# Kernel tuning notes

Hardware: AMD Instinct MI355X
Metric: run time of the kernel (lower is better)

The kernel has to match this reference:

```python
import jax, jax.numpy as jnp
import numpy as np

N = 50000      # nodes
E = 800000     # edges (before self-loops)
G = 128        # graphs in batch
IN = 128       # in_channels
HID = 32       # hidden_channels (per head)
HEADS = 4
OUT = 64       # out_channels
SLOPE = 0.2    # PyG GATConv default negative_slope


def setup_inputs() -> dict:
    key = jax.random.key(0)
    ks = jax.random.split(key, 24)
    s = 0.1
    inp = {
        'x': jax.random.normal(ks[0], (N, IN), jnp.float32),
        'edge_index': jax.random.randint(ks[1], (2, E), 0, N, dtype=jnp.int32),
        'batch': jnp.sort(jax.random.randint(ks[2], (N,), 0, G, dtype=jnp.int32)),
        # conv1: IN -> HEADS*HID, concat
        'W1': jax.random.normal(ks[3], (IN, HEADS * HID), jnp.float32) * s,
        'a1s': jax.random.normal(ks[4], (HEADS, HID), jnp.float32) * s,
        'a1d': jax.random.normal(ks[5], (HEADS, HID), jnp.float32) * s,
        'b1': jnp.zeros((HEADS * HID,), jnp.float32),
        # conv2: HEADS*HID -> HEADS*HID, concat
        'W2': jax.random.normal(ks[6], (HEADS * HID, HEADS * HID), jnp.float32) * s,
        'a2s': jax.random.normal(ks[7], (HEADS, HID), jnp.float32) * s,
        'a2d': jax.random.normal(ks[8], (HEADS, HID), jnp.float32) * s,
        'b2': jnp.zeros((HEADS * HID,), jnp.float32),
        # conv3
        'W3': jax.random.normal(ks[9], (HEADS * HID, HEADS * HID), jnp.float32) * s,
        'a3s': jax.random.normal(ks[10], (HEADS, HID), jnp.float32) * s,
        'a3d': jax.random.normal(ks[11], (HEADS, HID), jnp.float32) * s,
        'b3': jnp.zeros((HEADS * HID,), jnp.float32),
        # conv4: heads=1, concat=False -> HID
        'W4': jax.random.normal(ks[12], (HEADS * HID, 1 * HID), jnp.float32) * s,
        'a4s': jax.random.normal(ks[13], (1, HID), jnp.float32) * s,
        'a4d': jax.random.normal(ks[14], (1, HID), jnp.float32) * s,
        'b4': jnp.zeros((HID,), jnp.float32),
        # fc: HID -> OUT
        'fcW': jax.random.normal(ks[15], (HID, OUT), jnp.float32) * s,
        'fcb': jnp.zeros((OUT,), jnp.float32),
    }
    return inp


def gat_conv(x, src, dst, W, a_src, a_dst, bias, heads, ch, concat):
    # x: [N, F_in]; src/dst: [E'] with self-loops (PyG add_self_loops=True)
    h = (x @ W).reshape(N, heads, ch)                       # [N, H, C]
    alpha_s = jnp.einsum('nhc,hc->nh', h, a_src)            # [N, H]
    alpha_d = jnp.einsum('nhc,hc->nh', h, a_dst)
    e = jax.nn.leaky_relu(alpha_s[src] + alpha_d[dst], SLOPE)  # [E', H]
    # segment softmax over edges grouped by destination node
    e_max = jax.ops.segment_max(e, dst, num_segments=N)
    e = jnp.exp(e - e_max[dst])
    denom = jax.ops.segment_sum(e, dst, num_segments=N)
    alpha = e / (denom[dst] + 1e-16)                        # [E', H]
    msg = h[src] * alpha[:, :, None]                        # [E', H, C]
    out = jax.ops.segment_sum(msg, dst, num_segments=N)     # [N, H, C]
    out = out.reshape(N, heads * ch) if concat else out.mean(axis=1)
    return out + bias


def reference(x, edge_index, batch, W1, a1s, a1d, b1, W2, a2s, a2d, b2,
              W3, a3s, a3d, b3, W4, a4s, a4d, b4, fcW, fcb):
    loop = jnp.arange(N, dtype=edge_index.dtype)
    src = jnp.concatenate([edge_index[0], loop])            # add self-loops once
    dst = jnp.concatenate([edge_index[1], loop])
    h = jax.nn.elu(gat_conv(x, src, dst, W1, a1s, a1d, b1, HEADS, HID, True))
    h = jax.nn.elu(gat_conv(h, src, dst, W2, a2s, a2d, b2, HEADS, HID, True))
    h = jax.nn.elu(gat_conv(h, src, dst, W3, a3s, a3d, b3, HEADS, HID, True))
    h = jax.nn.elu(gat_conv(h, src, dst, W4, a4s, a4d, b4, 1, HID, False))
    # global mean pool over graphs
    counts = jax.ops.segment_sum(jnp.ones((N,), h.dtype), batch, num_segments=G)
    pooled = jax.ops.segment_sum(h, batch, num_segments=G) / jnp.maximum(counts, 1.0)[:, None]
    # dropout p=0.5 is identity at inference
    return pooled @ fcW + fcb                               # [G, OUT]
```

## Files before the change

kernel.cpp:

```cpp
#include <hip/hip_runtime.h>


constexpr int NN     = 50000;
constexpr int NNPAD  = 50048;
constexpr int EE     = 800000;
constexpr int ETOT   = EE + NN;
constexpr int GG     = 128;
constexpr int HIDC   = 32;
constexpr int OUTC   = 64;

constexpr int NRANGE = (NN + 127) / 128;
constexpr int EPB    = 4096;
constexpr int NBLK   = (EE + EPB - 1) / EPB;
constexpr int RCAP   = 2688;

typedef short  bf16x8 __attribute__((ext_vector_type(8)));
typedef float  f32x4  __attribute__((ext_vector_type(4)));

static __device__ __forceinline__ unsigned short f2bf(float f) {
    unsigned int u = __float_as_uint(f);
    unsigned int r = (u + 0x7fffu + ((u >> 16) & 1u)) >> 16;
    return (unsigned short)r;
}
static __device__ __forceinline__ float bflo(unsigned int v) {
    return __uint_as_float(v << 16);
}
static __device__ __forceinline__ float bfhi(unsigned int v) {
    return __uint_as_float(v & 0xffff0000u);
}

__global__ __launch_bounds__(256) void local_sort_kernel(
    const int* __restrict__ ei,
    unsigned int* __restrict__ blocksorted,
    int* __restrict__ boffs)
{
    __shared__ unsigned int sorted[EPB];
    __shared__ int hist[NRANGE + 1];
    __shared__ int scanv[NRANGE + 1];
    __shared__ int cur[NRANGE + 1];
    __shared__ int wsum4[4];
    __shared__ int ct_s;

    const int b = blockIdx.x, tid = threadIdx.x;
    const int lane = tid & 63, wid = tid >> 6;
    const int e0 = b * EPB;
    const int ecnt = min(EPB, EE - e0);

    for (int t = tid; t < NRANGE + 1; t += 256) hist[t] = 0;
    __syncthreads();

    unsigned int recs[16];
    int rkey[16];
#pragma unroll
    for (int k = 0; k < 16; ++k) {
        const int idx = tid + k * 256;
        rkey[k] = -1;
        if (idx < ecnt) {
            const int src = ei[e0 + idx];
            const int dst = ei[EE + e0 + idx];
            const int r = dst >> 7;
            recs[k] = (unsigned int)src | ((unsigned int)(dst & 127) << 16);
            rkey[k] = r;
            atomicAdd(&hist[r], 1);
        }
    }
    __syncthreads();

    int carry = 0;
    for (int base = 0; base < NRANGE + 1; base += 256) {
        const int i = base + tid;
        const int v = (i < NRANGE + 1) ? hist[i] : 0;
        int incl = v;
#pragma unroll
        for (int off = 1; off < 64; off <<= 1) {
            int t = __shfl_up(incl, off, 64);
            if (lane >= off) incl += t;
        }
        if (lane == 63) wsum4[wid] = incl;
        __syncthreads();
        if (tid == 0) {
            int s = 0;
#pragma unroll
            for (int w = 0; w < 4; ++w) { int t = wsum4[w]; wsum4[w] = s; s += t; }
            ct_s = s;
        }
        __syncthreads();
        const int excl = carry + wsum4[wid] + incl - v;
        if (i < NRANGE + 1) { scanv[i] = excl; cur[i] = excl; }
        carry += ct_s;
        __syncthreads();
    }

#pragma unroll
    for (int k = 0; k < 16; ++k) {
        if (rkey[k] >= 0) {
            const int pos = atomicAdd(&cur[rkey[k]], 1);
            sorted[pos] = recs[k];
        }
    }
    __syncthreads();

    for (int t = tid; t < ecnt; t += 256)
        blocksorted[(size_t)b * EPB + t] = sorted[t];
    for (int t = tid; t < NRANGE + 1; t += 256)
        boffs[b * (NRANGE + 1) + t] = scanv[t];
}

__global__ __launch_bounds__(512) void rbase_kernel(const int* __restrict__ boffs,
                                                    int* __restrict__ rbase)
{
    __shared__ int wsum[8], wpre[8];
    const int tid = threadIdx.x, lane = tid & 63, wid = tid >> 6;
    int tot = 0;
    if (tid < NRANGE) {
        for (int b = 0; b < NBLK; ++b) {
            const int* bp = boffs + b * (NRANGE + 1) + tid;
            tot += bp[1] - bp[0];
        }
        tot += min(128, NN - tid * 128);
    }
    int incl = tot;
#pragma unroll
    for (int off = 1; off < 64; off <<= 1) {
        int t = __shfl_up(incl, off, 64);
        if (lane >= off) incl += t;
    }
    if (lane == 63) wsum[wid] = incl;
    __syncthreads();
    if (tid < 8) {
        int wv = wsum[tid], winc = wv;
#pragma unroll
        for (int off = 1; off < 8; off <<= 1) {
            int t = __shfl_up(winc, off, 64);
            if (tid >= off) winc += t;
        }
        wpre[tid] = winc - wv;
    }
    __syncthreads();
    const int excl = wpre[wid] + incl - tot;
    if (tid < NRANGE) rbase[tid] = excl;
    if (tid == NRANGE - 1) rbase[NRANGE] = excl + tot;
}

__global__ __launch_bounds__(256) void phaseB_kernel(
    const int* __restrict__ boffs,
    const unsigned int* __restrict__ blocksorted,
    const int* __restrict__ rbase,
    int* __restrict__ offs,
    int* __restrict__ csrsrc)
{
    __shared__ unsigned int   rec[RCAP];
    __shared__ unsigned short outsrc[RCAP];
    __shared__ int runoff[NBLK + 1];
    __shared__ int bstart[NBLK];
    __shared__ int hist[128], lofs[128], cur[128];
    __shared__ int wsum4[4];
    __shared__ int tot0_s;

    const int r = blockIdx.x, tid = threadIdx.x;
    const int lane = tid & 63, wid = tid >> 6;
    const int base = r * 128;
    const int rn   = min(128, NN - base);

    int cnt = 0;
    if (tid < NBLK) {
        const int* bp = boffs + tid * (NRANGE + 1) + r;
        const int s = bp[0];
        bstart[tid] = s;
        cnt = bp[1] - s;
    }
    if (tid < 128) hist[tid] = 0;
    int incl = cnt;
#pragma unroll
    for (int off = 1; off < 64; off <<= 1) {
        int t = __shfl_up(incl, off, 64);
        if (lane >= off) incl += t;
    }
    if (lane == 63) wsum4[wid] = incl;
    __syncthreads();
    if (tid == 0) {
        int s = 0;
#pragma unroll
        for (int w = 0; w < 4; ++w) { int t = wsum4[w]; wsum4[w] = s; s += t; }
    }
    __syncthreads();
    const int excl = wsum4[wid] + incl - cnt;
    if (tid <= NBLK) runoff[tid] = excl;
    __syncthreads();

    const int tot8 = runoff[NBLK];
    for (int i = tid; i < tot8; i += 256) {
        int lo = 0, hi = NBLK;
        while (lo + 1 < hi) {
            const int mid = (lo + hi) >> 1;
            if (runoff[mid] <= i) lo = mid; else hi = mid;
        }
        rec[i] = blocksorted[(size_t)lo * EPB + bstart[lo] + (i - runoff[lo])];
    }
    for (int t = tid; t < rn; t += 256)
        rec[tot8 + t] = (unsigned int)(base + t) | ((unsigned int)t << 16);
    const int total = min(tot8 + rn, RCAP);
    __syncthreads();

    for (int t = tid; t < total; t += 256) atomicAdd(&hist[rec[t] >> 16], 1);
    __syncthreads();

    if (tid < 64) {
        int v = hist[tid], incl2 = v;
#pragma unroll
        for (int off = 1; off < 64; off <<= 1) {
            int t = __shfl_up(incl2, off, 64);
            if (tid >= off) incl2 += t;
        }
        lofs[tid] = incl2 - v;
        if (tid == 63) tot0_s = incl2;
    }
    __syncthreads();
    if (tid >= 64 && tid < 128) {
        const int l = tid & 63;
        int v = hist[tid], incl2 = v;
#pragma unroll
        for (int off = 1; off < 64; off <<= 1) {
            int t = __shfl_up(incl2, off, 64);
            if (l >= off) incl2 += t;
        }
        lofs[tid] = tot0_s + incl2 - v;
    }
    __syncthreads();

    if (tid < 128) cur[tid] = lofs[tid];
    if (tid < rn) offs[base + tid] = rbase[r] + lofs[tid];
    if (r == 0 && tid == 0) offs[NN] = rbase[NRANGE];
    __syncthreads();

    for (int t = tid; t < total; t += 256) {
        const unsigned int rc = rec[t];
        const int pos = atomicAdd(&cur[rc >> 16], 1);
        outsrc[pos] = (unsigned short)(rc & 0xffffu);
    }
    __syncthreads();
    const int rb = rbase[r];
    for (int t = tid; t < total; t += 256) csrsrc[rb + t] = (int)outsrc[t];
}

__global__ __launch_bounds__(256) void prep_kernel(
    const float* __restrict__ W1, const float* __restrict__ a1s, const float* __restrict__ a1d,
    const float* __restrict__ W2, const float* __restrict__ a2s, const float* __restrict__ a2d,
    const float* __restrict__ W3, const float* __restrict__ a3s, const float* __restrict__ a3d,
    const float* __restrict__ W4, const float* __restrict__ a4s, const float* __restrict__ a4d,
    unsigned short* __restrict__ wtg)
{
    __shared__ float ahat_s[128 * 8];
    const int l = blockIdx.x, tid = threadIdx.x;
    const float *W, *as_, *ad_;
    int fo, nh;
    if (l == 0)      { W = W1; as_ = a1s; ad_ = a1d; fo = 128; nh = 4; }
    else if (l == 1) { W = W2; as_ = a2s; ad_ = a2d; fo = 128; nh = 4; }
    else if (l == 2) { W = W3; as_ = a3s; ad_ = a3d; fo = 128; nh = 4; }
    else             { W = W4; as_ = a4s; ad_ = a4d; fo = 32;  nh = 1; }
    const int F_STG = fo + 16;

    for (int item = tid; item < 128 * 8; item += 256) {
        const int k = item >> 3, j = item & 7;
        const int hh = j & 3;
        const bool is_d = j >= 4;
        float v = 0.f;
        if (hh < nh) {
            const float* av = (is_d ? ad_ : as_) + hh * 32;
            const float* wp = W + (size_t)k * fo + hh * 32;
#pragma unroll 8
            for (int c = 0; c < 32; ++c) v = fmaf(wp[c], av[c], v);
        }
        ahat_s[item] = v;
    }
    __syncthreads();

    unsigned short* outb = wtg + (size_t)l * (144 * 128);
    for (int p = tid; p < F_STG * 64; p += 256) {
        const int n  = p % F_STG;
        const int k2 = p / F_STG;
        float w0 = 0.f, w1 = 0.f;
        if (n < fo) {
            w0 = W[(size_t)(2 * k2) * fo + n];
            w1 = W[(size_t)(2 * k2 + 1) * fo + n];
        } else {
            const int j = n - fo;
            if (j < 8) {
                w0 = ahat_s[(2 * k2) * 8 + j];
                w1 = ahat_s[(2 * k2 + 1) * 8 + j];
            }
        }
        const unsigned int packed = (unsigned int)f2bf(w0) | ((unsigned int)f2bf(w1) << 16);
        const int byte = n * 256 + ((4 * k2) ^ ((n & 7) << 4));
        *reinterpret_cast<unsigned int*>(reinterpret_cast<char*>(outb) + byte) = packed;
    }
}

__global__ void convert_x_kernel(const float* __restrict__ x, unsigned short* __restrict__ xb)
{
    int i = blockIdx.x * blockDim.x + threadIdx.x;
    if (i >= (NNPAD * 128) / 2) return;
    unsigned int packed = 0;
    if (2 * i < NN * 128) {
        float f0 = x[2 * i], f1 = x[2 * i + 1];
        packed = (unsigned int)f2bf(f0) | ((unsigned int)f2bf(f1) << 16);
    }
    reinterpret_cast<unsigned int*>(xb)[i] = packed;
}

template<int F_OUT, int NH>
__global__ __launch_bounds__(256) void gemm_mfma_kernel(
    const unsigned short* __restrict__ xb,
    const unsigned short* __restrict__ wtg,
    unsigned short* __restrict__ hb,
    float* __restrict__ as_out, float* __restrict__ ad_out)
{
    constexpr int F_STG = F_OUT + 16;
    __shared__ unsigned short wt[F_STG * 128];
    const int tid = threadIdx.x;

    {
        const bf16x8* __restrict__ wg = reinterpret_cast<const bf16x8*>(wtg);
        bf16x8* wl = reinterpret_cast<bf16x8*>(wt);
        constexpr int NV = F_STG * 16;
#pragma unroll
        for (int i = 0; i < NV / 256; ++i)
            wl[i * 256 + tid] = wg[i * 256 + tid];
    }
    __syncthreads();

    const int wave = tid >> 6, lane = tid & 63;
    const int row0 = blockIdx.x * 64 + wave * 16;
    const int arow = row0 + (lane & 15);
    const int kchunk = (lane >> 4) * 8;

    const unsigned short* __restrict__ ap = xb + (size_t)arow * 128;
    bf16x8 a[4];
#pragma unroll
    for (int ks = 0; ks < 4; ++ks)
        a[ks] = *reinterpret_cast<const bf16x8*>(ap + ks * 32 + kchunk);

    const int kb_base = (lane >> 4) * 16;
    const int rbase = row0 + (lane >> 4) * 4;

#pragma unroll
    for (int nt = 0; nt < F_OUT / 16; ++nt) {
        const int n = nt * 16 + (lane & 15);
        f32x4 acc = {0.f, 0.f, 0.f, 0.f};
#pragma unroll
        for (int ks = 0; ks < 4; ++ks) {
            const int byte = n * 256 + ((ks * 64 + kb_base) ^ ((n & 7) << 4));
            bf16x8 b = *reinterpret_cast<const bf16x8*>(
                reinterpret_cast<const char*>(wt) + byte);
            acc = __builtin_amdgcn_mfma_f32_16x16x32_bf16(a[ks], b, acc, 0, 0, 0);
        }
#pragma unroll
        for (int r = 0; r < 4; ++r)
            hb[(size_t)(rbase + r) * F_OUT + n] = f2bf(acc[r]);
    }

    {
        const int n = F_OUT + (lane & 15);
        f32x4 acc = {0.f, 0.f, 0.f, 0.f};
#pragma unroll
        for (int ks = 0; ks < 4; ++ks) {
            const int byte = n * 256 + ((ks * 64 + kb_base) ^ ((n & 7) << 4));
            bf16x8 b = *reinterpret_cast<const bf16x8*>(
                reinterpret_cast<const char*>(wt) + byte);
            acc = __builtin_amdgcn_mfma_f32_16x16x32_bf16(a[ks], b, acc, 0, 0, 0);
        }
        const int col = lane & 15;
        if (col < 8) {
            const int hh = col & 3;
            const bool is_d = col >= 4;
            if (hh < NH) {
                float* op = is_d ? ad_out : as_out;
#pragma unroll
                for (int r = 0; r < 4; ++r) {
                    const int row = rbase + r;
                    if (row < NN) {
                        if (NH == 4) op[row * 4 + hh] = acc[r];
                        else         op[row]          = acc[r];
                    }
                }
            }
        }
    }
}

template<int HEADS, int F_OUT, bool OUT_BF16>
__global__ __launch_bounds__(256) void aggregate_kernel(
    const unsigned short* __restrict__ hlin,
    const float* __restrict__ as_,
    const float* __restrict__ ad_,
    const int* __restrict__ offs,
    const int* __restrict__ csr_src,
    const float* __restrict__ bias,
    void* __restrict__ out_v)
{
    __shared__ float w_all[4][64 * HEADS];
    __shared__ int   s_all[4][64];
    const int wave = threadIdx.x >> 6;
    const int lane = threadIdx.x & 63;
    const int d    = blockIdx.x * 4 + wave;
    if (d >= NN) return;
    float* __restrict__ w_lds  = w_all[wave];
    int*   __restrict__ src_lds = s_all[wave];

    const int beg  = offs[d], end = offs[d + 1];
    const int deg  = end - beg;

    float ad_h[HEADS];
#pragma unroll
    for (int h = 0; h < HEADS; ++h) ad_h[h] = ad_[d * HEADS + h];

    float inv[HEADS];

    if (deg <= 64) {
        float ex[HEADS];
#pragma unroll
        for (int h = 0; h < HEADS; ++h) ex[h] = 0.f;
        int src = 0;
        if (lane < deg) {
            src = csr_src[beg + lane];
            if (HEADS == 4) {
                const float4 av = *reinterpret_cast<const float4*>(as_ + (size_t)src * 4);
                const float avv[4] = {av.x, av.y, av.z, av.w};
#pragma unroll
                for (int h = 0; h < 4; ++h) {
                    float e = avv[h] + ad_h[h];
                    e = fmaxf(e, 0.f) + 0.2f * fminf(e, 0.f);
                    ex[h] = __expf(e);
                }
            } else {
                float e = as_[src] + ad_h[0];
                e = fmaxf(e, 0.f) + 0.2f * fminf(e, 0.f);
                ex[0] = __expf(e);
            }
        }
        src_lds[lane] = src;
#pragma unroll
        for (int h = 0; h < HEADS; ++h) {
            float s = ex[h];
#pragma unroll
            for (int k = 1; k < 64; k <<= 1) s += __shfl_xor(s, k, 64);
            inv[h] = 1.f / (s + 1e-16f);
            w_lds[lane * HEADS + h] = ex[h] * inv[h];
        }
        asm volatile("s_waitcnt lgkmcnt(0)" ::: "memory");
    } else {
        float ssum[HEADS];
#pragma unroll
        for (int h = 0; h < HEADS; ++h) ssum[h] = 0.f;
        for (int p = beg + lane; p < end; p += 64) {
            const int src = csr_src[p];
            if (HEADS == 4) {
                const float4 av = *reinterpret_cast<const float4*>(as_ + (size_t)src * 4);
                const float avv[4] = {av.x, av.y, av.z, av.w};
#pragma unroll
                for (int h = 0; h < 4; ++h) {
                    float e = avv[h] + ad_h[h];
                    e = fmaxf(e, 0.f) + 0.2f * fminf(e, 0.f);
                    ssum[h] += __expf(e);
                }
            } else {
                float e = as_[src] + ad_h[0];
                e = fmaxf(e, 0.f) + 0.2f * fminf(e, 0.f);
                ssum[0] += __expf(e);
            }
        }
#pragma unroll
        for (int h = 0; h < HEADS; ++h) {
            float s = ssum[h];
#pragma unroll
            for (int k = 1; k < 64; k <<= 1) s += __shfl_xor(s, k, 64);
            inv[h] = 1.f / (s + 1e-16f);
        }
    }

    float acc[4] = {0.f, 0.f, 0.f, 0.f};

    for (int base = beg; base < end; base += 64) {
        const int cnt = min(64, end - base);
        if (deg > 64) {
            const int p = base + lane;
            int src = 0;
            float w[HEADS];
#pragma unroll
            for (int h = 0; h < HEADS; ++h) w[h] = 0.f;
            if (p < end) {
                src = csr_src[p];
                if (HEADS == 4) {
                    const float4 av = *reinterpret_cast<const float4*>(as_ + (size_t)src * 4);
                    const float avv[4] = {av.x, av.y, av.z, av.w};
#pragma unroll
                    for (int h = 0; h < 4; ++h) {
                        float e = avv[h] + ad_h[h];
                        e = fmaxf(e, 0.f) + 0.2f * fminf(e, 0.f);
                        w[h] = __expf(e) * inv[h];
                    }
                } else {
                    float e = as_[src] + ad_h[0];
                    e = fmaxf(e, 0.f) + 0.2f * fminf(e, 0.f);
                    w[0] = __expf(e) * inv[0];
                }
            }
            src_lds[lane] = src;
#pragma unroll
            for (int h = 0; h < HEADS; ++h) w_lds[lane * HEADS + h] = w[h];
            asm volatile("s_waitcnt lgkmcnt(0)" ::: "memory");
        }

        if (F_OUT == 128) {
            const int half = lane >> 5, cl = lane & 31;
            const int cntR = (cnt + 1) & ~1;
#pragma unroll 4
            for (int j = 0; j < cntR; j += 2) {
                const int   srcj = src_lds[j + half];
                const float w    = w_lds[(j + half) * 4 + (cl >> 3)];
                const uint2 hv   = *reinterpret_cast<const uint2*>(
                    hlin + (size_t)srcj * 128 + cl * 4);
                acc[0] = fmaf(w, bflo(hv.x), acc[0]);
                acc[1] = fmaf(w, bfhi(hv.x), acc[1]);
                acc[2] = fmaf(w, bflo(hv.y), acc[2]);
                acc[3] = fmaf(w, bfhi(hv.y), acc[3]);
            }
        } else {
            const int q = lane >> 4, cl = lane & 15;
            const int cntR = (cnt + 3) & ~3;
#pragma unroll 4
            for (int j = 0; j < cntR; j += 4) {
                const int   srcj = src_lds[j + q];
                const float w    = w_lds[j + q];
                const unsigned int hv = *reinterpret_cast<const unsigned int*>(
                    hlin + (size_t)srcj * 32 + cl * 2);
                acc[0] = fmaf(w, bflo(hv), acc[0]);
                acc[1] = fmaf(w, bfhi(hv), acc[1]);
            }
        }
    }

    if (F_OUT == 128) {
#pragma unroll
        for (int t = 0; t < 4; ++t) acc[t] += __shfl_xor(acc[t], 32, 64);
        if (lane < 32) {
            const int c0 = lane * 4;
            float v[4];
#pragma unroll
            for (int t = 0; t < 4; ++t) {
                float v0 = acc[t] + bias[c0 + t];
                v[t] = (v0 > 0.f) ? v0 : (__expf(v0) - 1.f);
            }
            unsigned int p0 = (unsigned int)f2bf(v[0]) | ((unsigned int)f2bf(v[1]) << 16);
            unsigned int p1 = (unsigned int)f2bf(v[2]) | ((unsigned int)f2bf(v[3]) << 16);
            uint2* op = reinterpret_cast<uint2*>(
                (unsigned short*)out_v + (size_t)d * 128 + c0);
            *op = make_uint2(p0, p1);
        }
    } else {
        acc[0] += __shfl_xor(acc[0], 16, 64); acc[0] += __shfl_xor(acc[0], 32, 64);
        acc[1] += __shfl_xor(acc[1], 16, 64); acc[1] += __shfl_xor(acc[1], 32, 64);
        if (lane < 16) {
            const int c0 = lane * 2;
            float v0 = acc[0] + bias[c0];
            float v1 = acc[1] + bias[c0 + 1];
            v0 = (v0 > 0.f) ? v0 : (__expf(v0) - 1.f);
            v1 = (v1 > 0.f) ? v1 : (__expf(v1) - 1.f);
            if (OUT_BF16) {
                unsigned int pk = (unsigned int)f2bf(v0) | ((unsigned int)f2bf(v1) << 16);
                reinterpret_cast<unsigned int*>(out_v)[(size_t)d * 16 + lane] = pk;
            } else {
                reinterpret_cast<float2*>(out_v)[(size_t)d * 16 + lane] =
                    make_float2(v0, v1);
            }
        }
    }
}

__global__ __launch_bounds__(256) void pool_fc_kernel(
    const float* __restrict__ h4, const int* __restrict__ batch,
    const float* __restrict__ fcW, const float* __restrict__ fcb,
    float* __restrict__ out)
{
    const int g = blockIdx.x;
    __shared__ int sb, se;
    if (threadIdx.x == 0) {
        int lo = 0, hi = NN;
        while (lo < hi) { int mid = (lo + hi) >> 1; if (batch[mid] < g) lo = mid + 1; else hi = mid; }
        sb = lo;
        lo = sb; hi = NN;
        while (lo < hi) { int mid = (lo + hi) >> 1; if (batch[mid] < g + 1) lo = mid + 1; else hi = mid; }
        se = lo;
    }
    __syncthreads();
    const int s = sb, e = se;

    const int c  = threadIdx.x & 31;
    const int rg = threadIdx.x >> 5;
    float acc = 0.f;
    for (int n = s + rg; n < e; n += 8)
        acc += h4[(size_t)n * HIDC + c];

    __shared__ float red[8][32];
    red[rg][c] = acc;
    __syncthreads();
    __shared__ float pooled_s[32];
    if (threadIdx.x < 32) {
        float v = 0.f;
#pragma unroll
        for (int r = 0; r < 8; ++r) v += red[r][threadIdx.x];
        pooled_s[threadIdx.x] = v / fmaxf((float)(e - s), 1.f);
    }
    __syncthreads();
    if (threadIdx.x < OUTC) {
        const int o = threadIdx.x;
        float a2 = fcb[o];
#pragma unroll
        for (int cc = 0; cc < HIDC; ++cc)
            a2 = fmaf(pooled_s[cc], fcW[cc * OUTC + o], a2);
        out[g * OUTC + o] = a2;
    }
}

extern "C" void kernel_launch(void* const* d_in, const int* in_sizes, int n_in,
                              void* d_out, int out_size, void* d_ws, size_t ws_size,
                              hipStream_t stream)
{
    const float* x     = (const float*)d_in[0];
    const int*   ei    = (const int*)d_in[1];
    const int*   batch = (const int*)d_in[2];
    const float* W1  = (const float*)d_in[3];
    const float* a1s = (const float*)d_in[4];
    const float* a1d = (const float*)d_in[5];
    const float* b1  = (const float*)d_in[6];
    const float* W2  = (const float*)d_in[7];
    const float* a2s = (const float*)d_in[8];
    const float* a2d = (const float*)d_in[9];
    const float* b2  = (const float*)d_in[10];
    const float* W3  = (const float*)d_in[11];
    const float* a3s = (const float*)d_in[12];
    const float* a3d = (const float*)d_in[13];
    const float* b3  = (const float*)d_in[14];
    const float* W4  = (const float*)d_in[15];
    const float* a4s = (const float*)d_in[16];
    const float* a4d = (const float*)d_in[17];
    const float* b4  = (const float*)d_in[18];
    const float* fcW = (const float*)d_in[19];
    const float* fcb = (const float*)d_in[20];
    float* out = (float*)d_out;

    unsigned short* xb = (unsigned short*)d_ws;
    unsigned short* hb = xb + (size_t)NNPAD * 128;
    float* asb  = (float*)(hb + (size_t)NNPAD * 128);
    float* adb  = asb + (size_t)NN * 4;
    int*   offs   = (int*)(adb + (size_t)NN * 4);
    int*   csrsrc = offs + NN + 1;
    int*   boffs  = csrsrc + ETOT;
    int*   rbase  = boffs + NBLK * (NRANGE + 1);
    unsigned short* wtg = (unsigned short*)(rbase + NRANGE + 1);
    unsigned int* blocksorted = (unsigned int*)hb;
    float* bufF = (float*)xb;

    local_sort_kernel<<<NBLK, 256, 0, stream>>>(ei, blocksorted, boffs);
    rbase_kernel<<<1, 512, 0, stream>>>(boffs, rbase);
    phaseB_kernel<<<NRANGE, 256, 0, stream>>>(boffs, blocksorted, rbase, offs, csrsrc);

    prep_kernel<<<4, 256, 0, stream>>>(W1, a1s, a1d, W2, a2s, a2d,
                                       W3, a3s, a3d, W4, a4s, a4d, wtg);
    convert_x_kernel<<<(NNPAD * 64 + 255) / 256, 256, 0, stream>>>(x, xb);

    constexpr int GEMM_GRID = NNPAD / 64;
    constexpr int AGG_GRID  = (NN + 3) / 4;
    constexpr size_t WSTRIDE = 144 * 128;

    gemm_mfma_kernel<128, 4><<<GEMM_GRID, 256, 0, stream>>>(xb, wtg + 0 * WSTRIDE, hb, asb, adb);
    aggregate_kernel<4, 128, true><<<AGG_GRID, 256, 0, stream>>>(hb, asb, adb, offs, csrsrc, b1, xb);
    gemm_mfma_kernel<128, 4><<<GEMM_GRID, 256, 0, stream>>>(xb, wtg + 1 * WSTRIDE, hb, asb, adb);
    aggregate_kernel<4, 128, true><<<AGG_GRID, 256, 0, stream>>>(hb, asb, adb, offs, csrsrc, b2, xb);
    gemm_mfma_kernel<128, 4><<<GEMM_GRID, 256, 0, stream>>>(xb, wtg + 2 * WSTRIDE, hb, asb, adb);
    aggregate_kernel<4, 128, true><<<AGG_GRID, 256, 0, stream>>>(hb, asb, adb, offs, csrsrc, b3, xb);
    gemm_mfma_kernel<32, 1><<<GEMM_GRID, 256, 0, stream>>>(xb, wtg + 3 * WSTRIDE, hb, asb, adb);
    aggregate_kernel<1, 32, false><<<AGG_GRID, 256, 0, stream>>>(hb, asb, adb, offs, csrsrc, b4, bufF);

    pool_fc_kernel<<<GG, 256, 0, stream>>>(bufF, batch, fcW, fcb, out);
}
```

Before: 266.4 us.

## Fuse x conversion into GEMM, parallelize range totals, widen aggregate gathers

The separate fp32-to-bf16 conversion kernel is removed; the first GEMM now reads fp32 x directly and converts in registers. Each GEMM block now covers 128 rows over two passes, which halves the grid and amortises the weight staging in LDS. The serial per-range total loop in rbase is split into a parallel rtot kernel (one wave per range, reduced with shuffles) followed by a scan kernel. The aggregation gathers switch to 16-byte loads, with 8 accumulators per lane and more edges processed in parallel per wave, at the cost of more padded slots and extra shuffle reductions.

```diff
diff --git a/kernel.cpp b/kernel.cpp
--- a/kernel.cpp
+++ b/kernel.cpp
@@ -27,6 +27,9 @@
 }
 static __device__ __forceinline__ float bfhi(unsigned int v) {
     return __uint_as_float(v & 0xffff0000u);
+}
+static __device__ __forceinline__ float elu(float v) {
+    return (v > 0.f) ? v : (__expf(v) - 1.f);
 }
 
 __global__ __launch_bounds__(256) void local_sort_kernel(
@@ -106,19 +109,28 @@
         boffs[b * (NRANGE + 1) + t] = scanv[t];
 }
 
-__global__ __launch_bounds__(512) void rbase_kernel(const int* __restrict__ boffs,
+__global__ __launch_bounds__(256) void rtot_kernel(const int* __restrict__ boffs,
+                                                   int* __restrict__ rtot)
+{
+    const int r = blockIdx.x * 4 + (threadIdx.x >> 6);
+    const int lane = threadIdx.x & 63;
+    if (r >= NRANGE) return;
+    int tot = 0;
+    for (int b = lane; b < NBLK; b += 64) {
+        const int* bp = boffs + b * (NRANGE + 1) + r;
+        tot += bp[1] - bp[0];
+    }
+#pragma unroll
+    for (int k = 1; k < 64; k <<= 1) tot += __shfl_xor(tot, k, 64);
+    if (lane == 0) rtot[r] = tot + min(128, NN - r * 128);
+}
+
+__global__ __launch_bounds__(512) void rscan_kernel(const int* __restrict__ rtot,
                                                     int* __restrict__ rbase)
 {
     __shared__ int wsum[8], wpre[8];
     const int tid = threadIdx.x, lane = tid & 63, wid = tid >> 6;
-    int tot = 0;
-    if (tid < NRANGE) {
-        for (int b = 0; b < NBLK; ++b) {
-            const int* bp = boffs + b * (NRANGE + 1) + tid;
-            tot += bp[1] - bp[0];
-        }
-        tot += min(128, NN - tid * 128);
-    }
+    int tot = (tid < NRANGE) ? rtot[tid] : 0;
     int incl = tot;
 #pragma unroll
     for (int off = 1; off < 64; off <<= 1) {
@@ -296,21 +308,9 @@
     }
 }
 
-__global__ void convert_x_kernel(const float* __restrict__ x, unsigned short* __restrict__ xb)
-{
-    int i = blockIdx.x * blockDim.x + threadIdx.x;
-    if (i >= (NNPAD * 128) / 2) return;
-    unsigned int packed = 0;
-    if (2 * i < NN * 128) {
-        float f0 = x[2 * i], f1 = x[2 * i + 1];
-        packed = (unsigned int)f2bf(f0) | ((unsigned int)f2bf(f1) << 16);
-    }
-    reinterpret_cast<unsigned int*>(xb)[i] = packed;
-}
-
-template<int F_OUT, int NH>
+template<int F_OUT, int NH, bool XF32>
 __global__ __launch_bounds__(256) void gemm_mfma_kernel(
-    const unsigned short* __restrict__ xb,
+    const void* __restrict__ xv,
     const unsigned short* __restrict__ wtg,
     unsigned short* __restrict__ hb,
     float* __restrict__ as_out, float* __restrict__ ad_out)
@@ -330,57 +330,85 @@
     __syncthreads();
 
     const int wave = tid >> 6, lane = tid & 63;
-    const int row0 = blockIdx.x * 64 + wave * 16;
-    const int arow = row0 + (lane & 15);
     const int kchunk = (lane >> 4) * 8;
-
-    const unsigned short* __restrict__ ap = xb + (size_t)arow * 128;
-    bf16x8 a[4];
-#pragma unroll
-    for (int ks = 0; ks < 4; ++ks)
-        a[ks] = *reinterpret_cast<const bf16x8*>(ap + ks * 32 + kchunk);
-
     const int kb_base = (lane >> 4) * 16;
-    const int rbase = row0 + (lane >> 4) * 4;
-
-#pragma unroll
-    for (int nt = 0; nt < F_OUT / 16; ++nt) {
-        const int n = nt * 16 + (lane & 15);
-        f32x4 acc = {0.f, 0.f, 0.f, 0.f};
-#pragma unroll
-        for (int ks = 0; ks < 4; ++ks) {
-            const int byte = n * 256 + ((ks * 64 + kb_base) ^ ((n & 7) << 4));
-            bf16x8 b = *reinterpret_cast<const bf16x8*>(
-                reinterpret_cast<const char*>(wt) + byte);
-            acc = __builtin_amdgcn_mfma_f32_16x16x32_bf16(a[ks], b, acc, 0, 0, 0);
-        }
-#pragma unroll
-        for (int r = 0; r < 4; ++r)
-            hb[(size_t)(rbase + r) * F_OUT + n] = f2bf(acc[r]);
-    }
-
-    {
-        const int n = F_OUT + (lane & 15);
-        f32x4 acc = {0.f, 0.f, 0.f, 0.f};
-#pragma unroll
-        for (int ks = 0; ks < 4; ++ks) {
-            const int byte = n * 256 + ((ks * 64 + kb_base) ^ ((n & 7) << 4));
-            bf16x8 b = *reinterpret_cast<const bf16x8*>(
-                reinterpret_cast<const char*>(wt) + byte);
-            acc = __builtin_amdgcn_mfma_f32_16x16x32_bf16(a[ks], b, acc, 0, 0, 0);
-        }
-        const int col = lane & 15;
-        if (col < 8) {
-            const int hh = col & 3;
-            const bool is_d = col >= 4;
-            if (hh < NH) {
-                float* op = is_d ? ad_out : as_out;
-#pragma unroll
-                for (int r = 0; r < 4; ++r) {
-                    const int row = rbase + r;
-                    if (row < NN) {
-                        if (NH == 4) op[row * 4 + hh] = acc[r];
-                        else         op[row]          = acc[r];
+
+#pragma unroll
+    for (int rr = 0; rr < 2; ++rr) {
+        const int row0 = blockIdx.x * 128 + rr * 64 + wave * 16;
+        const int arow = row0 + (lane & 15);
+
+        bf16x8 a[4];
+        if (XF32) {
+            if (arow < NN) {
+                const float* __restrict__ ap = (const float*)xv + (size_t)arow * 128;
+#pragma unroll
+                for (int ks = 0; ks < 4; ++ks) {
+                    const float4 f0 = *reinterpret_cast<const float4*>(ap + ks * 32 + kchunk);
+                    const float4 f1 = *reinterpret_cast<const float4*>(ap + ks * 32 + kchunk + 4);
+                    bf16x8 v;
+                    v[0] = (short)f2bf(f0.x); v[1] = (short)f2bf(f0.y);
+                    v[2] = (short)f2bf(f0.z); v[3] = (short)f2bf(f0.w);
+                    v[4] = (short)f2bf(f1.x); v[5] = (short)f2bf(f1.y);
+                    v[6] = (short)f2bf(f1.z); v[7] = (short)f2bf(f1.w);
+                    a[ks] = v;
+                }
+            } else {
+#pragma unroll
+                for (int ks = 0; ks < 4; ++ks) a[ks] = bf16x8{0,0,0,0,0,0,0,0};
+            }
+        } else {
+            const unsigned short* __restrict__ ap =
+                (const unsigned short*)xv + (size_t)arow * 128;
+#pragma unroll
+            for (int ks = 0; ks < 4; ++ks)
+                a[ks] = *reinterpret_cast<const bf16x8*>(ap + ks * 32 + kchunk);
+        }
+
+        const int rbase = row0 + (lane >> 4) * 4;
+
+#pragma unroll
+        for (int nt = 0; nt < F_OUT / 16; ++nt) {
+            const int n = nt * 16 + (lane & 15);
+            f32x4 acc = {0.f, 0.f, 0.f, 0.f};
+#pragma unroll
+            for (int ks = 0; ks < 4; ++ks) {
+                const int byte = n * 256 + ((ks * 64 + kb_base) ^ ((n & 7) << 4));
+                bf16x8 b = *reinterpret_cast<const bf16x8*>(
+                    reinterpret_cast<const char*>(wt) + byte);
+                acc = __builtin_amdgcn_mfma_f32_16x16x32_bf16(a[ks], b, acc, 0, 0, 0);
+            }
+#pragma unroll
+            for (int r = 0; r < 4; ++r) {
+                const int row = rbase + r;
+                if (row < NN)
+                    hb[(size_t)row * F_OUT + n] = f2bf(acc[r]);
+            }
+        }
+
+        {
+            const int n = F_OUT + (lane & 15);
+            f32x4 acc = {0.f, 0.f, 0.f, 0.f};
+#pragma unroll
+            for (int ks = 0; ks < 4; ++ks) {
+                const int byte = n * 256 + ((ks * 64 + kb_base) ^ ((n & 7) << 4));
+                bf16x8 b = *reinterpret_cast<const bf16x8*>(
+                    reinterpret_cast<const char*>(wt) + byte);
+                acc = __builtin_amdgcn_mfma_f32_16x16x32_bf16(a[ks], b, acc, 0, 0, 0);
+            }
+            const int col = lane & 15;
+            if (col < 8) {
+                const int hh = col & 3;
+                const bool is_d = col >= 4;
+                if (hh < NH) {
+                    float* op = is_d ? ad_out : as_out;
+#pragma unroll
+                    for (int r = 0; r < 4; ++r) {
+                        const int row = rbase + r;
+                        if (row < NN) {
+                            if (NH == 4) op[row * 4 + hh] = acc[r];
+                            else         op[row]          = acc[r];
+                        }
                     }
                 }
             }
@@ -478,7 +506,10 @@
         }
     }
 
-    float acc[4] = {0.f, 0.f, 0.f, 0.f};
+    float acc[8] = {0.f, 0.f, 0.f, 0.f, 0.f, 0.f, 0.f, 0.f};
+    const int q  = (F_OUT == 128) ? (lane >> 4) : (lane >> 2);
+    const int cl = (F_OUT == 128) ? (lane & 15) : (lane & 3);
+    const int hd = (F_OUT == 128) ? (cl >> 2) : 0;
 
     for (int base = beg; base < end; base += 64) {
         const int cnt = min(64, end - base);
@@ -512,67 +543,78 @@
         }
 
         if (F_OUT == 128) {
-            const int half = lane >> 5, cl = lane & 31;
-            const int cntR = (cnt + 1) & ~1;
-#pragma unroll 4
-            for (int j = 0; j < cntR; j += 2) {
-                const int   srcj = src_lds[j + half];
-                const float w    = w_lds[(j + half) * 4 + (cl >> 3)];
-                const uint2 hv   = *reinterpret_cast<const uint2*>(
-                    hlin + (size_t)srcj * 128 + cl * 4);
+            const int cntR = (cnt + 3) & ~3;
+#pragma unroll 2
+            for (int j = 0; j < cntR; j += 4) {
+                const int   slot = j + q;
+                const int   srcj = src_lds[slot];
+                const float w    = w_lds[slot * 4 + hd];
+                const uint4 hv   = *reinterpret_cast<const uint4*>(
+                    hlin + (size_t)srcj * 128 + cl * 8);
                 acc[0] = fmaf(w, bflo(hv.x), acc[0]);
                 acc[1] = fmaf(w, bfhi(hv.x), acc[1]);
                 acc[2] = fmaf(w, bflo(hv.y), acc[2]);
                 acc[3] = fmaf(w, bfhi(hv.y), acc[3]);
+                acc[4] = fmaf(w, bflo(hv.z), acc[4]);
+                acc[5] = fmaf(w, bfhi(hv.z), acc[5]);
+                acc[6] = fmaf(w, bflo(hv.w), acc[6]);
+                acc[7] = fmaf(w, bfhi(hv.w), acc[7]);
             }
         } else {
-            const int q = lane >> 4, cl = lane & 15;
-            const int cntR = (cnt + 3) & ~3;
-#pragma unroll 4
-            for (int j = 0; j < cntR; j += 4) {
-                const int   srcj = src_lds[j + q];
-                const float w    = w_lds[j + q];
-                const unsigned int hv = *reinterpret_cast<const unsigned int*>(
-                    hlin + (size_t)srcj * 32 + cl * 2);
-                acc[0] = fmaf(w, bflo(hv), acc[0]);
-                acc[1] = fmaf(w, bfhi(hv), acc[1]);
+            const int cntR = (cnt + 15) & ~15;
+#pragma unroll 2
+            for (int j = 0; j < cntR; j += 16) {
+                const int   slot = j + q;
+                const int   srcj = src_lds[slot];
+                const float w    = w_lds[slot];
+                const uint4 hv   = *reinterpret_cast<const uint4*>(
+                    hlin + (size_t)srcj * 32 + cl * 8);
+                acc[0] = fmaf(w, bflo(hv.x), acc[0]);
+                acc[1] = fmaf(w, bfhi(hv.x), acc[1]);
+                acc[2] = fmaf(w, bflo(hv.y), acc[2]);
+                acc[3] = fmaf(w, bfhi(hv.y), acc[3]);
+                acc[4] = fmaf(w, bflo(hv.z), acc[4]);
+                acc[5] = fmaf(w, bfhi(hv.z), acc[5]);
+                acc[6] = fmaf(w, bflo(hv.w), acc[6]);
+                acc[7] = fmaf(w, bfhi(hv.w), acc[7]);
             }
         }
     }
 
     if (F_OUT == 128) {
 #pragma unroll
-        for (int t = 0; t < 4; ++t) acc[t] += __shfl_xor(acc[t], 32, 64);
-        if (lane < 32) {
-            const int c0 = lane * 4;
-            float v[4];
-#pragma unroll
-            for (int t = 0; t < 4; ++t) {
-                float v0 = acc[t] + bias[c0 + t];
-                v[t] = (v0 > 0.f) ? v0 : (__expf(v0) - 1.f);
-            }
-            unsigned int p0 = (unsigned int)f2bf(v[0]) | ((unsigned int)f2bf(v[1]) << 16);
-            unsigned int p1 = (unsigned int)f2bf(v[2]) | ((unsigned int)f2bf(v[3]) << 16);
-            uint2* op = reinterpret_cast<uint2*>(
-                (unsigned short*)out_v + (size_t)d * 128 + c0);
-            *op = make_uint2(p0, p1);
+        for (int t = 0; t < 8; ++t) {
+            acc[t] += __shfl_xor(acc[t], 16, 64);
+            acc[t] += __shfl_xor(acc[t], 32, 64);
+        }
+        if (lane < 16) {
+            const int c0 = lane * 8;
+            float v[8];
+#pragma unroll
+            for (int t = 0; t < 8; ++t) v[t] = elu(acc[t] + bias[c0 + t]);
+            uint4 pk;
+            pk.x = (unsigned int)f2bf(v[0]) | ((unsigned int)f2bf(v[1]) << 16);
+            pk.y = (unsigned int)f2bf(v[2]) | ((unsigned int)f2bf(v[3]) << 16);
+            pk.z = (unsigned int)f2bf(v[4]) | ((unsigned int)f2bf(v[5]) << 16);
+            pk.w = (unsigned int)f2bf(v[6]) | ((unsigned int)f2bf(v[7]) << 16);
+            *reinterpret_cast<uint4*>((unsigned short*)out_v + (size_t)d * 128 + c0) = pk;
         }
     } else {
-        acc[0] += __shfl_xor(acc[0], 16, 64); acc[0] += __shfl_xor(acc[0], 32, 64);
-        acc[1] += __shfl_xor(acc[1], 16, 64); acc[1] += __shfl_xor(acc[1], 32, 64);
-        if (lane < 16) {
-            const int c0 = lane * 2;
-            float v0 = acc[0] + bias[c0];
-            float v1 = acc[1] + bias[c0 + 1];
-            v0 = (v0 > 0.f) ? v0 : (__expf(v0) - 1.f);
-            v1 = (v1 > 0.f) ? v1 : (__expf(v1) - 1.f);
-            if (OUT_BF16) {
-                unsigned int pk = (unsigned int)f2bf(v0) | ((unsigned int)f2bf(v1) << 16);
-                reinterpret_cast<unsigned int*>(out_v)[(size_t)d * 16 + lane] = pk;
-            } else {
-                reinterpret_cast<float2*>(out_v)[(size_t)d * 16 + lane] =
-                    make_float2(v0, v1);
-            }
+#pragma unroll
+        for (int t = 0; t < 8; ++t) {
+            acc[t] += __shfl_xor(acc[t], 4, 64);
+            acc[t] += __shfl_xor(acc[t], 8, 64);
+            acc[t] += __shfl_xor(acc[t], 16, 64);
+            acc[t] += __shfl_xor(acc[t], 32, 64);
+        }
+        if (lane < 4) {
+            const int c0 = lane * 8;
+            float v[8];
+#pragma unroll
+            for (int t = 0; t < 8; ++t) v[t] = elu(acc[t] + bias[c0 + t]);
+            float* op = (float*)out_v + (size_t)d * 32 + c0;
+            *reinterpret_cast<float4*>(op)     = make_float4(v[0], v[1], v[2], v[3]);
+            *reinterpret_cast<float4*>(op + 4) = make_float4(v[4], v[5], v[6], v[7]);
         }
     }
 }
@@ -657,29 +699,30 @@
     int*   csrsrc = offs + NN + 1;
     int*   boffs  = csrsrc + ETOT;
     int*   rbase  = boffs + NBLK * (NRANGE + 1);
-    unsigned short* wtg = (unsigned short*)(rbase + NRANGE + 1);
+    int*   rtot   = rbase + NRANGE + 1;
+    unsigned short* wtg = (unsigned short*)(rtot + NRANGE);
     unsigned int* blocksorted = (unsigned int*)hb;
     float* bufF = (float*)xb;
 
     local_sort_kernel<<<NBLK, 256, 0, stream>>>(ei, blocksorted, boffs);
-    rbase_kernel<<<1, 512, 0, stream>>>(boffs, rbase);
+    rtot_kernel<<<(NRANGE + 3) / 4, 256, 0, stream>>>(boffs, rtot);
+    rscan_kernel<<<1, 512, 0, stream>>>(rtot, rbase);
     phaseB_kernel<<<NRANGE, 256, 0, stream>>>(boffs, blocksorted, rbase, offs, csrsrc);
 
     prep_kernel<<<4, 256, 0, stream>>>(W1, a1s, a1d, W2, a2s, a2d,
                                        W3, a3s, a3d, W4, a4s, a4d, wtg);
-    convert_x_kernel<<<(NNPAD * 64 + 255) / 256, 256, 0, stream>>>(x, xb);
-
-    constexpr int GEMM_GRID = NNPAD / 64;
+
+    constexpr int GEMM_GRID = NNPAD / 128;
     constexpr int AGG_GRID  = (NN + 3) / 4;
     constexpr size_t WSTRIDE = 144 * 128;
 
-    gemm_mfma_kernel<128, 4><<<GEMM_GRID, 256, 0, stream>>>(xb, wtg + 0 * WSTRIDE, hb, asb, adb);
+    gemm_mfma_kernel<128, 4, true><<<GEMM_GRID, 256, 0, stream>>>(x, wtg + 0 * WSTRIDE, hb, asb, adb);
     aggregate_kernel<4, 128, true><<<AGG_GRID, 256, 0, stream>>>(hb, asb, adb, offs, csrsrc, b1, xb);
-    gemm_mfma_kernel<128, 4><<<GEMM_GRID, 256, 0, stream>>>(xb, wtg + 1 * WSTRIDE, hb, asb, adb);
+    gemm_mfma_kernel<128, 4, false><<<GEMM_GRID, 256, 0, stream>>>(xb, wtg + 1 * WSTRIDE, hb, asb, adb);
     aggregate_kernel<4, 128, true><<<AGG_GRID, 256, 0, stream>>>(hb, asb, adb, offs, csrsrc, b2, xb);
-    gemm_mfma_kernel<128, 4><<<GEMM_GRID, 256, 0, stream>>>(xb, wtg + 2 * WSTRIDE, hb, asb, adb);
+    gemm_mfma_kernel<128, 4, false><<<GEMM_GRID, 256, 0, stream>>>(xb, wtg + 2 * WSTRIDE, hb, asb, adb);
     aggregate_kernel<4, 128, true><<<AGG_GRID, 256, 0, stream>>>(hb, asb, adb, offs, csrsrc, b3, xb);
-    gemm_mfma_kernel<32, 1><<<GEMM_GRID, 256, 0, stream>>>(xb, wtg + 3 * WSTRIDE, hb, asb, adb);
+    gemm_mfma_kernel<32, 1, false><<<GEMM_GRID, 256, 0, stream>>>(xb, wtg + 3 * WSTRIDE, hb, asb, adb);
     aggregate_kernel<1, 32, false><<<AGG_GRID, 256, 0, stream>>>(hb, asb, adb, offs, csrsrc, b4, bufF);
 
     pool_fc_kernel<<<GG, 256, 0, stream>>>(bufF, batch, fcW, fcb, out);
```

Measured after the change: 260.1 us. -2.4%, faster.
